# Optimization experiments

Measured on AMD Instinct MI355X. Metric: run time of the kernel, lower is better.

## Reference

```python
import jax, jax.numpy as jnp
import numpy as np

D_MODEL, D_FFN, N_EXPERTS, TOP_K = 1024, 4096, 8, 2
BATCH, SEQ = 4, 1024


def setup_inputs() -> dict:
    key = jax.random.key(0)
    kx, kr, k1, k2, k3 = jax.random.split(key, 5)
    scale = 0.02
    return {
        "x": jax.random.normal(kx, (BATCH, SEQ, D_MODEL), dtype=jnp.float32),
        "w_router": jax.random.normal(kr, (D_MODEL, N_EXPERTS), dtype=jnp.float32) * scale,
        "w1": jax.random.normal(k1, (N_EXPERTS, D_MODEL, D_FFN), dtype=jnp.float32) * scale,
        "w2": jax.random.normal(k2, (N_EXPERTS, D_FFN, D_MODEL), dtype=jnp.float32) * scale,
        "w3": jax.random.normal(k3, (N_EXPERTS, D_MODEL, D_FFN), dtype=jnp.float32) * scale,
    }


def reference(x, w_router, w1, w2, w3):
    B, S, D = x.shape
    E = w_router.shape[1]
    T = B * S
    xf = x.reshape(T, D)

    # --- router: softmax over experts, top-k, renormalize ---
    router_probs = jax.nn.softmax(xf @ w_router, axis=-1)          # (T, E)
    topk_probs, topk_idx = jax.lax.top_k(router_probs, TOP_K)      # (T, K)
    topk_probs = topk_probs / topk_probs.sum(axis=-1, keepdims=True)

    # per-token combine weight for each expert (top_k indices are distinct,
    # matching the torch per-slot accumulation exactly)
    comb = jnp.zeros((T, E), dtype=xf.dtype)
    comb = comb.at[jnp.arange(T)[:, None], topk_idx].add(topk_probs)  # (T, E)

    # --- dense SwiGLU experts (same math as masked loop) ---
    h = jnp.einsum("td,edf->tef", xf, w1)                          # (T, E, F)
    g = jnp.einsum("td,edf->tef", xf, w3)                          # (T, E, F)
    y = jnp.einsum("tef,efd->ted", jax.nn.silu(h) * g, w2)         # (T, E, D)
    out = jnp.einsum("te,ted->td", comb, y).reshape(B, S, D)

    # --- load-balance aux loss ---
    expert_mask = jax.nn.one_hot(topk_idx, E, dtype=jnp.float32).sum(axis=1)  # (T, E)
    tokens_per_expert = expert_mask.sum(axis=0) / T
    mean_probs = router_probs.mean(axis=0)
    aux_loss = E * jnp.sum(tokens_per_expert * mean_probs)
    return out, aux_loss
```

## Files before the change

kernel.cpp:

```cpp
#include <hip/hip_runtime.h>
#include <hip/hip_bf16.h>
#include <cstdint>
#include <cstddef>

#define TT 4096
#define DM 1024
#define DF 4096
#define NE 8
#define BTAB 72

typedef __attribute__((ext_vector_type(8))) short bf16x8;
typedef __attribute__((ext_vector_type(8))) unsigned short ushort8;
typedef __attribute__((ext_vector_type(4))) float f32x4;

static __device__ __forceinline__ unsigned short f2bf(float f) {
    union { float f; unsigned int u; } v; v.f = f;
    unsigned int u = v.u;
    return (unsigned short)((u + 0x7FFFu + ((u >> 16) & 1u)) >> 16);
}
static __device__ __forceinline__ float bf2f(unsigned short h) {
    union { unsigned int u; float f; } v; v.u = ((unsigned int)h) << 16;
    return v.f;
}

#define GLOAD16(gsrc, ldst)                                                        \
    __builtin_amdgcn_global_load_lds(                                              \
        (const __attribute__((address_space(1))) void*)(gsrc),                     \
        (__attribute__((address_space(3))) void*)(ldst), 16, 0, 0)

__global__ void transpose_to_bf16(const float* __restrict__ in,
                                  unsigned short* __restrict__ out,
                                  int R, int C) {
    __shared__ float tile[32][33];
    const int e = blockIdx.z;
    const float* src = in + (size_t)e * R * C;
    unsigned short* dst = out + (size_t)e * R * C;
    const int c0 = blockIdx.x * 32, r0 = blockIdx.y * 32;
    const int tx = threadIdx.x, ty = threadIdx.y;
    #pragma unroll
    for (int i = 0; i < 4; ++i) {
        int r = r0 + ty + i * 8;
        tile[ty + i * 8][tx] = src[(size_t)r * C + c0 + tx];
    }
    __syncthreads();
    #pragma unroll
    for (int i = 0; i < 4; ++i) {
        int c = c0 + ty + i * 8;
        dst[(size_t)c * R + r0 + tx] = f2bf(tile[tx][ty + i * 8]);
    }
}

__global__ void router_kernel(const float* __restrict__ x,
                              const float* __restrict__ wr,
                              unsigned short* __restrict__ xb,
                              int* __restrict__ topi, float* __restrict__ topw,
                              float* __restrict__ probsum) {
    __shared__ float s_ps[NE];
    const int tid = threadIdx.x;
    if (tid < NE) s_ps[tid] = 0.f;
    __syncthreads();
    const int wid = tid >> 6, lane = tid & 63;
    const int t = blockIdx.x * 4 + wid;
    float acc[NE] = {0.f, 0.f, 0.f, 0.f, 0.f, 0.f, 0.f, 0.f};
    const float* xr = x + (size_t)t * DM;
    unsigned short* xbr = xb + (size_t)t * DM;
    for (int it = 0; it < DM / 64; ++it) {
        int d = it * 64 + lane;
        float xv = xr[d];
        xbr[d] = f2bf(xv);
        const float* w = wr + d * NE;
        #pragma unroll
        for (int e = 0; e < NE; ++e) acc[e] = fmaf(xv, w[e], acc[e]);
    }
    #pragma unroll
    for (int e = 0; e < NE; ++e) {
        float v = acc[e];
        #pragma unroll
        for (int off = 32; off; off >>= 1) v += __shfl_xor(v, off);
        acc[e] = v;
    }
    if (lane == 0) {
        float m = acc[0];
        #pragma unroll
        for (int e = 1; e < NE; ++e) m = fmaxf(m, acc[e]);
        float p[NE], s = 0.f;
        #pragma unroll
        for (int e = 0; e < NE; ++e) { p[e] = expf(acc[e] - m); s += p[e]; }
        float inv = 1.f / s;
        #pragma unroll
        for (int e = 0; e < NE; ++e) { p[e] *= inv; atomicAdd(&s_ps[e], p[e]); }
        int i1 = 0; float p1 = p[0];
        #pragma unroll
        for (int e = 1; e < NE; ++e) if (p[e] > p1) { p1 = p[e]; i1 = e; }
        int i2 = -1; float p2 = -1.f;
        #pragma unroll
        for (int e = 0; e < NE; ++e) if (e != i1 && p[e] > p2) { p2 = p[e]; i2 = e; }
        float rs = 1.f / (p1 + p2);
        topi[t * 2] = i1; topi[t * 2 + 1] = i2;
        topw[t * 2] = p1 * rs; topw[t * 2 + 1] = p2 * rs;
    }
    __syncthreads();
    if (tid < NE) atomicAdd(&probsum[tid], s_ps[tid]);
}

__global__ void assign_kernel(const int* __restrict__ topi,
                              int* __restrict__ list, int* __restrict__ slotpos,
                              int* __restrict__ cnt) {
    const int e = blockIdx.x;
    __shared__ int s_wc[4];
    const int tid = threadIdx.x, wid = tid >> 6, lane = tid & 63;
    int running = 0;
    for (int base = 0; base < TT; base += 256) {
        int t = base + tid;
        int hit = 0, slot = 0;
        int a = topi[2 * t], b = topi[2 * t + 1];
        if (a == e) { hit = 1; slot = 0; }
        else if (b == e) { hit = 1; slot = 1; }
        unsigned long long m = __ballot(hit);
        if (lane == 0) s_wc[wid] = __popcll(m);
        __syncthreads();
        int pre = 0, tot = 0;
        #pragma unroll
        for (int q = 0; q < 4; ++q) { int c = s_wc[q]; tot += c; if (q < wid) pre += c; }
        if (hit) {
            int pos = running + pre + __popcll(m & ((1ull << lane) - 1ull));
            list[e * TT + pos] = t;
            slotpos[2 * t + slot] = pos;
        }
        running += tot;
        __syncthreads();
    }
    if (tid == 0) cnt[e] = running;
}

__global__ void finalize_kernel(const int* __restrict__ cnt,
                                const float* __restrict__ probsum,
                                int* __restrict__ offs,
                                unsigned int* __restrict__ blocktab,
                                float* __restrict__ out_aux) {
    int o = 0;
    float aux = 0.f;
    int nb = 0;
    for (int e = 0; e < NE; ++e) {
        offs[e] = o; o += cnt[e];
        aux += (float)cnt[e] * probsum[e];
        int nrb = (cnt[e] + 127) >> 7;
        for (int rb = 0; rb < nrb; ++rb) blocktab[nb++] = ((unsigned)e << 16) | rb;
    }
    while (nb < BTAB) blocktab[nb++] = 0xFFFFFFFFu;
    *out_aux = (float)NE * aux / ((float)TT * (float)TT);
}

static __device__ __forceinline__ const bf16x8* frag_ptr(
        const unsigned short* base, int row, int ph16) {
    return (const bf16x8*)((const char*)base + row * 64 + ph16);
}

__global__ __launch_bounds__(256, 2) void gemm1_kernel(
    const unsigned short* __restrict__ xb,
    const unsigned short* __restrict__ w1T,
    const unsigned short* __restrict__ w3T,
    unsigned short* __restrict__ act,
    const int* __restrict__ list,
    const int* __restrict__ cnt,
    const int* __restrict__ offs,
    const unsigned int* __restrict__ blocktab) {
    const unsigned int tab = blocktab[blockIdx.y];
    if (tab == 0xFFFFFFFFu) return;
    const int e = tab >> 16;
    const int rowbase = (int)(tab & 0xFFFFu) << 7;
    const int ce = cnt[e];
    const int fbase = blockIdx.x * 128;

    __shared__ __align__(16) unsigned short As[128 * 32];
    __shared__ __align__(16) unsigned short B1s[128 * 32];
    __shared__ __align__(16) unsigned short B3s[128 * 32];

    const int tid = threadIdx.x;
    const int lrow = tid >> 2;
    const int q = (tid & 3) ^ ((tid >> 3) & 3);

    int sp0 = rowbase + lrow;       if (sp0 >= ce) sp0 = ce - 1;
    int sp1 = rowbase + 64 + lrow;  if (sp1 >= ce) sp1 = ce - 1;
    const size_t tok0 = (size_t)list[e * TT + sp0];
    const size_t tok1 = (size_t)list[e * TT + sp1];

    const unsigned short* a0 = xb + tok0 * DM + q * 8;
    const unsigned short* a1 = xb + tok1 * DM + q * 8;
    const unsigned short* b1a = w1T + ((size_t)e * DF + fbase + lrow) * DM + q * 8;
    const unsigned short* b1b = b1a + (size_t)64 * DM;
    const unsigned short* b3a = w3T + ((size_t)e * DF + fbase + lrow) * DM + q * 8;
    const unsigned short* b3b = b3a + (size_t)64 * DM;

    char* ldsA  = (char*)As  + tid * 16;
    char* ldsB1 = (char*)B1s + tid * 16;
    char* ldsB3 = (char*)B3s + tid * 16;

    const int wid = tid >> 6, lane = tid & 63;
    const int wm = wid >> 1, wn = wid & 1;
    const int g = lane >> 4, r = lane & 15;
    const int ph16 = (g ^ ((r >> 1) & 3)) << 4;

    f32x4 acch[4][4] = {};
    f32x4 accg[4][4] = {};

    for (int k0 = 0; k0 < DM; k0 += 32) {
        GLOAD16(a0 + k0,  ldsA);
        GLOAD16(a1 + k0,  ldsA + 4096);
        GLOAD16(b1a + k0, ldsB1);
        GLOAD16(b1b + k0, ldsB1 + 4096);
        GLOAD16(b3a + k0, ldsB3);
        GLOAD16(b3b + k0, ldsB3 + 4096);
        __syncthreads();
        bf16x8 af[4];
        #pragma unroll
        for (int m = 0; m < 4; ++m)
            af[m] = *frag_ptr(As, wm * 64 + m * 16 + r, ph16);
        #pragma unroll
        for (int n = 0; n < 4; ++n) {
            bf16x8 f1 = *frag_ptr(B1s, wn * 64 + n * 16 + r, ph16);
            bf16x8 f3 = *frag_ptr(B3s, wn * 64 + n * 16 + r, ph16);
            #pragma unroll
            for (int m = 0; m < 4; ++m) {
                acch[m][n] = __builtin_amdgcn_mfma_f32_16x16x32_bf16(af[m], f1, acch[m][n], 0, 0, 0);
                accg[m][n] = __builtin_amdgcn_mfma_f32_16x16x32_bf16(af[m], f3, accg[m][n], 0, 0, 0);
            }
        }
        __syncthreads();
    }

    const int ob = offs[e];
    #pragma unroll
    for (int m = 0; m < 4; ++m) {
        #pragma unroll
        for (int j = 0; j < 4; ++j) {
            const int pos = rowbase + wm * 64 + m * 16 + g * 4 + j;
            if (pos < ce) {
                unsigned short* arow = act + (size_t)(ob + pos) * DF + fbase + wn * 64;
                #pragma unroll
                for (int n = 0; n < 4; ++n) {
                    float h = acch[m][n][j];
                    float gv = accg[m][n][j];
                    float a = (h / (1.f + __expf(-h))) * gv;
                    arow[n * 16 + r] = f2bf(a);
                }
            }
        }
    }
}

__global__ __launch_bounds__(256, 2) void gemm2_kernel(
    const unsigned short* __restrict__ act,
    const unsigned short* __restrict__ w2T,
    unsigned short* __restrict__ ybuf,
    const int* __restrict__ cnt,
    const int* __restrict__ offs,
    const unsigned int* __restrict__ blocktab) {
    const unsigned int tab = blocktab[blockIdx.y];
    if (tab == 0xFFFFFFFFu) return;
    const int e = tab >> 16;
    const int rowbase = (int)(tab & 0xFFFFu) << 7;
    const int ce = cnt[e];
    const int dbase = blockIdx.x * 128;
    const int ob = offs[e];

    __shared__ __align__(16) unsigned short As[128 * 32];
    __shared__ __align__(16) unsigned short Bs[128 * 32];

    const int tid = threadIdx.x;
    const int lrow = tid >> 2;
    const int q = (tid & 3) ^ ((tid >> 3) & 3);

    int sp0 = rowbase + lrow;       if (sp0 >= ce) sp0 = ce - 1;
    int sp1 = rowbase + 64 + lrow;  if (sp1 >= ce) sp1 = ce - 1;

    const unsigned short* a0 = act + (size_t)(ob + sp0) * DF + q * 8;
    const unsigned short* a1 = act + (size_t)(ob + sp1) * DF + q * 8;
    const unsigned short* b0 = w2T + ((size_t)e * DM + dbase + lrow) * DF + q * 8;
    const unsigned short* b1 = b0 + (size_t)64 * DF;

    char* ldsA = (char*)As + tid * 16;
    char* ldsB = (char*)Bs + tid * 16;

    const int wid = tid >> 6, lane = tid & 63;
    const int wm = wid >> 1, wn = wid & 1;
    const int g = lane >> 4, r = lane & 15;
    const int ph16 = (g ^ ((r >> 1) & 3)) << 4;

    f32x4 acc[4][4] = {};

    for (int k0 = 0; k0 < DF; k0 += 32) {
        GLOAD16(a0 + k0, ldsA);
        GLOAD16(a1 + k0, ldsA + 4096);
        GLOAD16(b0 + k0, ldsB);
        GLOAD16(b1 + k0, ldsB + 4096);
        __syncthreads();
        bf16x8 af[4];
        #pragma unroll
        for (int m = 0; m < 4; ++m)
            af[m] = *frag_ptr(As, wm * 64 + m * 16 + r, ph16);
        #pragma unroll
        for (int n = 0; n < 4; ++n) {
            bf16x8 bfr = *frag_ptr(Bs, wn * 64 + n * 16 + r, ph16);
            #pragma unroll
            for (int m = 0; m < 4; ++m)
                acc[m][n] = __builtin_amdgcn_mfma_f32_16x16x32_bf16(af[m], bfr, acc[m][n], 0, 0, 0);
        }
        __syncthreads();
    }

    #pragma unroll
    for (int m = 0; m < 4; ++m) {
        #pragma unroll
        for (int j = 0; j < 4; ++j) {
            const int pos = rowbase + wm * 64 + m * 16 + g * 4 + j;
            if (pos < ce) {
                unsigned short* yrow = ybuf + (size_t)(ob + pos) * DM + dbase + wn * 64;
                #pragma unroll
                for (int n = 0; n < 4; ++n)
                    yrow[n * 16 + r] = f2bf(acc[m][n][j]);
            }
        }
    }
}

__global__ void combine_kernel(const unsigned short* __restrict__ ybuf,
                               const int* __restrict__ topi,
                               const float* __restrict__ topw,
                               const int* __restrict__ slotpos,
                               const int* __restrict__ offs,
                               float* __restrict__ out) {
    const int t = blockIdx.x;
    const int tid = threadIdx.x;
    const int e0 = topi[2 * t], e1 = topi[2 * t + 1];
    const int r0 = offs[e0] + slotpos[2 * t];
    const int r1 = offs[e1] + slotpos[2 * t + 1];
    const float w0 = topw[2 * t], w1 = topw[2 * t + 1];
    ushort4 a = *(const ushort4*)(ybuf + (size_t)r0 * DM + tid * 4);
    ushort4 b = *(const ushort4*)(ybuf + (size_t)r1 * DM + tid * 4);
    float4 o;
    o.x = w0 * bf2f(a.x) + w1 * bf2f(b.x);
    o.y = w0 * bf2f(a.y) + w1 * bf2f(b.y);
    o.z = w0 * bf2f(a.z) + w1 * bf2f(b.z);
    o.w = w0 * bf2f(a.w) + w1 * bf2f(b.w);
    *(float4*)(out + (size_t)t * DM + tid * 4) = o;
}

extern "C" void kernel_launch(void* const* d_in, const int* in_sizes, int n_in,
                              void* d_out, int out_size, void* d_ws, size_t ws_size,
                              hipStream_t stream) {
    (void)in_sizes; (void)n_in; (void)ws_size;
    const float* x  = (const float*)d_in[0];
    const float* wr = (const float*)d_in[1];
    const float* w1 = (const float*)d_in[2];
    const float* w2 = (const float*)d_in[3];
    const float* w3 = (const float*)d_in[4];
    float* out = (float*)d_out;

    char* ws = (char*)d_ws;
    size_t off = 0;
    auto alloc = [&](size_t bytes) -> void* {
        void* p = ws + off;
        off = (off + bytes + 255) & ~(size_t)255;
        return p;
    };
    unsigned short* w1T = (unsigned short*)alloc((size_t)NE * DF * DM * 2);
    unsigned short* w3T = (unsigned short*)alloc((size_t)NE * DF * DM * 2);
    unsigned short* w2T = (unsigned short*)alloc((size_t)NE * DM * DF * 2);
    unsigned short* act = (unsigned short*)alloc((size_t)2 * TT * DF * 2);
    unsigned short* xb  = (unsigned short*)alloc((size_t)TT * DM * 2);
    int*   topi    = (int*)alloc(TT * 2 * sizeof(int));
    float* topw    = (float*)alloc(TT * 2 * sizeof(float));
    int*   list    = (int*)alloc((size_t)NE * TT * sizeof(int));
    int*   slotpos = (int*)alloc(TT * 2 * sizeof(int));
    int*   cnt     = (int*)alloc(NE * sizeof(int));
    int*   offs    = (int*)alloc(NE * sizeof(int));
    float* probsum = (float*)alloc(NE * sizeof(float));
    unsigned int* blocktab = (unsigned int*)alloc(BTAB * sizeof(unsigned int));
    unsigned short* ybuf = w1T;

    hipMemsetAsync(probsum, 0, NE * sizeof(float), stream);

    dim3 tb(32, 8);
    transpose_to_bf16<<<dim3(DF / 32, DM / 32, NE), tb, 0, stream>>>(w1, w1T, DM, DF);
    transpose_to_bf16<<<dim3(DF / 32, DM / 32, NE), tb, 0, stream>>>(w3, w3T, DM, DF);
    transpose_to_bf16<<<dim3(DM / 32, DF / 32, NE), tb, 0, stream>>>(w2, w2T, DF, DM);

    router_kernel<<<TT / 4, 256, 0, stream>>>(x, wr, xb, topi, topw, probsum);
    assign_kernel<<<NE, 256, 0, stream>>>(topi, list, slotpos, cnt);
    finalize_kernel<<<1, 1, 0, stream>>>(cnt, probsum, offs, blocktab, out + (out_size - 1));

    gemm1_kernel<<<dim3(DF / 128, BTAB), 256, 0, stream>>>(xb, w1T, w3T, act, list, cnt, offs, blocktab);
    gemm2_kernel<<<dim3(DM / 128, BTAB), 256, 0, stream>>>(act, w2T, ybuf, cnt, offs, blocktab);
    combine_kernel<<<TT, 256, 0, stream>>>(ybuf, topi, topw, slotpos, offs, out);
}
```

Baseline: 481.4 us.

## Triple-buffer GEMM K-loops with async LDS loads and vectorize weight transpose

Both expert GEMMs now use a three-stage LDS ring buffer. Global-to-LDS loads for tile t+2 are issued before computing tile t, and explicit vmcnt waits plus barriers replace the two __syncthreads per iteration, so memory latency can overlap with MFMA work. gemm2's launch bounds go up to 3 blocks per CU. The weight transpose/bf16 conversion kernel moves to 64x64 tiles with float4 loads and 16-byte ushort8 stores. The extra LDS (48KB for gemm1) can cut occupancy, and the hand-counted vmcnt values must stay correct for the number of loads per stage.

```diff
diff --git a/kernel.cpp b/kernel.cpp
--- a/kernel.cpp
+++ b/kernel.cpp
@@ -28,25 +28,34 @@
         (const __attribute__((address_space(1))) void*)(gsrc),                     \
         (__attribute__((address_space(3))) void*)(ldst), 16, 0, 0)
 
-__global__ void transpose_to_bf16(const float* __restrict__ in,
-                                  unsigned short* __restrict__ out,
-                                  int R, int C) {
-    __shared__ float tile[32][33];
+__global__ void transpose_v2(const float* __restrict__ in,
+                             unsigned short* __restrict__ out,
+                             int R, int C) {
+    __shared__ float tile[64][65];
     const int e = blockIdx.z;
     const float* src = in + (size_t)e * R * C;
     unsigned short* dst = out + (size_t)e * R * C;
-    const int c0 = blockIdx.x * 32, r0 = blockIdx.y * 32;
-    const int tx = threadIdx.x, ty = threadIdx.y;
+    const int c0 = blockIdx.x * 64, r0 = blockIdx.y * 64;
+    const int tid = threadIdx.x;
     #pragma unroll
     for (int i = 0; i < 4; ++i) {
-        int r = r0 + ty + i * 8;
-        tile[ty + i * 8][tx] = src[(size_t)r * C + c0 + tx];
+        int idx = tid + i * 256;
+        int rr = idx >> 4, cc = idx & 15;
+        float4 v = *(const float4*)(src + (size_t)(r0 + rr) * C + c0 + cc * 4);
+        tile[rr][cc * 4 + 0] = v.x;
+        tile[rr][cc * 4 + 1] = v.y;
+        tile[rr][cc * 4 + 2] = v.z;
+        tile[rr][cc * 4 + 3] = v.w;
     }
     __syncthreads();
     #pragma unroll
-    for (int i = 0; i < 4; ++i) {
-        int c = c0 + ty + i * 8;
-        dst[(size_t)c * R + r0 + tx] = f2bf(tile[tx][ty + i * 8]);
+    for (int i = 0; i < 2; ++i) {
+        int idx = tid + i * 256;
+        int c = idx >> 3, rc = idx & 7;
+        ushort8 o;
+        #pragma unroll
+        for (int j = 0; j < 8; ++j) o[j] = f2bf(tile[rc * 8 + j][c]);
+        *(ushort8*)(dst + (size_t)(c0 + c) * R + r0 + rc * 8) = o;
     }
 }
 
@@ -156,6 +165,13 @@
     return (const bf16x8*)((const char*)base + row * 64 + ph16);
 }
 
+#define WAITBAR(N)                                                \
+    asm volatile("s_waitcnt vmcnt(" #N ")" ::: "memory");         \
+    __builtin_amdgcn_s_barrier();
+#define ENDBAR                                                    \
+    asm volatile("" ::: "memory");                                \
+    __builtin_amdgcn_s_barrier();
+
 __global__ __launch_bounds__(256, 2) void gemm1_kernel(
     const unsigned short* __restrict__ xb,
     const unsigned short* __restrict__ w1T,
@@ -172,9 +188,9 @@
     const int ce = cnt[e];
     const int fbase = blockIdx.x * 128;
 
-    __shared__ __align__(16) unsigned short As[128 * 32];
-    __shared__ __align__(16) unsigned short B1s[128 * 32];
-    __shared__ __align__(16) unsigned short B3s[128 * 32];
+    __shared__ __align__(16) unsigned short As[3 * 128 * 32];
+    __shared__ __align__(16) unsigned short B1s[3 * 128 * 32];
+    __shared__ __align__(16) unsigned short B3s[3 * 128 * 32];
 
     const int tid = threadIdx.x;
     const int lrow = tid >> 2;
@@ -204,30 +220,50 @@
     f32x4 acch[4][4] = {};
     f32x4 accg[4][4] = {};
 
-    for (int k0 = 0; k0 < DM; k0 += 32) {
-        GLOAD16(a0 + k0,  ldsA);
-        GLOAD16(a1 + k0,  ldsA + 4096);
-        GLOAD16(b1a + k0, ldsB1);
-        GLOAD16(b1b + k0, ldsB1 + 4096);
-        GLOAD16(b3a + k0, ldsB3);
-        GLOAD16(b3b + k0, ldsB3 + 4096);
-        __syncthreads();
-        bf16x8 af[4];
-        #pragma unroll
-        for (int m = 0; m < 4; ++m)
-            af[m] = *frag_ptr(As, wm * 64 + m * 16 + r, ph16);
-        #pragma unroll
-        for (int n = 0; n < 4; ++n) {
-            bf16x8 f1 = *frag_ptr(B1s, wn * 64 + n * 16 + r, ph16);
-            bf16x8 f3 = *frag_ptr(B3s, wn * 64 + n * 16 + r, ph16);
-            #pragma unroll
-            for (int m = 0; m < 4; ++m) {
-                acch[m][n] = __builtin_amdgcn_mfma_f32_16x16x32_bf16(af[m], f1, acch[m][n], 0, 0, 0);
-                accg[m][n] = __builtin_amdgcn_mfma_f32_16x16x32_bf16(af[m], f3, accg[m][n], 0, 0, 0);
-            }
-        }
-        __syncthreads();
-    }
+#define STAGE1(T, BUF)                                   \
+    {   const int koff = (T) * 32;                       \
+        const int bo = (BUF) * 8192;                     \
+        GLOAD16(a0 + koff,  ldsA + bo);                  \
+        GLOAD16(a1 + koff,  ldsA + bo + 4096);           \
+        GLOAD16(b1a + koff, ldsB1 + bo);                 \
+        GLOAD16(b1b + koff, ldsB1 + bo + 4096);          \
+        GLOAD16(b3a + koff, ldsB3 + bo);                 \
+        GLOAD16(b3b + koff, ldsB3 + bo + 4096); }
+
+#define COMP1(BS)                                                           \
+    {   const unsigned short* Ac  = As  + (BS) * 4096;                      \
+        const unsigned short* B1c = B1s + (BS) * 4096;                      \
+        const unsigned short* B3c = B3s + (BS) * 4096;                      \
+        bf16x8 af[4];                                                       \
+        _Pragma("unroll") for (int m = 0; m < 4; ++m)                       \
+            af[m] = *frag_ptr(Ac, wm * 64 + m * 16 + r, ph16);              \
+        _Pragma("unroll") for (int n = 0; n < 4; ++n) {                     \
+            bf16x8 f1 = *frag_ptr(B1c, wn * 64 + n * 16 + r, ph16);         \
+            bf16x8 f3 = *frag_ptr(B3c, wn * 64 + n * 16 + r, ph16);         \
+            _Pragma("unroll") for (int m = 0; m < 4; ++m) {                 \
+                acch[m][n] = __builtin_amdgcn_mfma_f32_16x16x32_bf16(af[m], f1, acch[m][n], 0, 0, 0); \
+                accg[m][n] = __builtin_amdgcn_mfma_f32_16x16x32_bf16(af[m], f3, accg[m][n], 0, 0, 0); } } }
+
+    const int NT = DM / 32;
+    STAGE1(0, 0);
+    STAGE1(1, 1);
+    int bs = 0, sb = 2;
+    for (int t = 0; t < NT - 2; ++t) {
+        STAGE1(t + 2, sb);
+        WAITBAR(12)
+        COMP1(bs)
+        ENDBAR
+        bs = (bs + 1 == 3) ? 0 : bs + 1;
+        sb = (sb + 1 == 3) ? 0 : sb + 1;
+    }
+    WAITBAR(6)
+    COMP1(bs)
+    ENDBAR
+    bs = (bs + 1 == 3) ? 0 : bs + 1;
+    WAITBAR(0)
+    COMP1(bs)
+#undef STAGE1
+#undef COMP1
 
     const int ob = offs[e];
     #pragma unroll
@@ -249,7 +285,7 @@
     }
 }
 
-__global__ __launch_bounds__(256, 2) void gemm2_kernel(
+__global__ __launch_bounds__(256, 3) void gemm2_kernel(
     const unsigned short* __restrict__ act,
     const unsigned short* __restrict__ w2T,
     unsigned short* __restrict__ ybuf,
@@ -264,8 +300,8 @@
     const int dbase = blockIdx.x * 128;
     const int ob = offs[e];
 
-    __shared__ __align__(16) unsigned short As[128 * 32];
-    __shared__ __align__(16) unsigned short Bs[128 * 32];
+    __shared__ __align__(16) unsigned short As[3 * 128 * 32];
+    __shared__ __align__(16) unsigned short Bs[3 * 128 * 32];
 
     const int tid = threadIdx.x;
     const int lrow = tid >> 2;
@@ -289,25 +325,45 @@
 
     f32x4 acc[4][4] = {};
 
-    for (int k0 = 0; k0 < DF; k0 += 32) {
-        GLOAD16(a0 + k0, ldsA);
-        GLOAD16(a1 + k0, ldsA + 4096);
-        GLOAD16(b0 + k0, ldsB);
-        GLOAD16(b1 + k0, ldsB + 4096);
-        __syncthreads();
-        bf16x8 af[4];
-        #pragma unroll
-        for (int m = 0; m < 4; ++m)
-            af[m] = *frag_ptr(As, wm * 64 + m * 16 + r, ph16);
-        #pragma unroll
-        for (int n = 0; n < 4; ++n) {
-            bf16x8 bfr = *frag_ptr(Bs, wn * 64 + n * 16 + r, ph16);
-            #pragma unroll
-            for (int m = 0; m < 4; ++m)
-                acc[m][n] = __builtin_amdgcn_mfma_f32_16x16x32_bf16(af[m], bfr, acc[m][n], 0, 0, 0);
-        }
-        __syncthreads();
-    }
+#define STAGE2(T, BUF)                                   \
+    {   const int koff = (T) * 32;                       \
+        const int bo = (BUF) * 8192;                     \
+        GLOAD16(a0 + koff, ldsA + bo);                   \
+        GLOAD16(a1 + koff, ldsA + bo + 4096);            \
+        GLOAD16(b0 + koff, ldsB + bo);                   \
+        GLOAD16(b1 + koff, ldsB + bo + 4096); }
+
+#define COMP2(BS)                                                           \
+    {   const unsigned short* Ac = As + (BS) * 4096;                        \
+        const unsigned short* Bc = Bs + (BS) * 4096;                        \
+        bf16x8 af[4];                                                       \
+        _Pragma("unroll") for (int m = 0; m < 4; ++m)                       \
+            af[m] = *frag_ptr(Ac, wm * 64 + m * 16 + r, ph16);              \
+        _Pragma("unroll") for (int n = 0; n < 4; ++n) {                     \
+            bf16x8 bfr = *frag_ptr(Bc, wn * 64 + n * 16 + r, ph16);         \
+            _Pragma("unroll") for (int m = 0; m < 4; ++m)                   \
+                acc[m][n] = __builtin_amdgcn_mfma_f32_16x16x32_bf16(af[m], bfr, acc[m][n], 0, 0, 0); } }
+
+    const int NT = DF / 32;
+    STAGE2(0, 0);
+    STAGE2(1, 1);
+    int bs = 0, sb = 2;
+    for (int t = 0; t < NT - 2; ++t) {
+        STAGE2(t + 2, sb);
+        WAITBAR(8)
+        COMP2(bs)
+        ENDBAR
+        bs = (bs + 1 == 3) ? 0 : bs + 1;
+        sb = (sb + 1 == 3) ? 0 : sb + 1;
+    }
+    WAITBAR(4)
+    COMP2(bs)
+    ENDBAR
+    bs = (bs + 1 == 3) ? 0 : bs + 1;
+    WAITBAR(0)
+    COMP2(bs)
+#undef STAGE2
+#undef COMP2
 
     #pragma unroll
     for (int m = 0; m < 4; ++m) {
@@ -381,10 +437,10 @@
 
     hipMemsetAsync(probsum, 0, NE * sizeof(float), stream);
 
-    dim3 tb(32, 8);
-    transpose_to_bf16<<<dim3(DF / 32, DM / 32, NE), tb, 0, stream>>>(w1, w1T, DM, DF);
-    transpose_to_bf16<<<dim3(DF / 32, DM / 32, NE), tb, 0, stream>>>(w3, w3T, DM, DF);
-    transpose_to_bf16<<<dim3(DM / 32, DF / 32, NE), tb, 0, stream>>>(w2, w2T, DF, DM);
+    dim3 tb(256);
+    transpose_v2<<<dim3(DF / 64, DM / 64, NE), tb, 0, stream>>>(w1, w1T, DM, DF);
+    transpose_v2<<<dim3(DF / 64, DM / 64, NE), tb, 0, stream>>>(w3, w3T, DM, DF);
+    transpose_v2<<<dim3(DM / 64, DF / 64, NE), tb, 0, stream>>>(w2, w2T, DF, DM);
 
     router_kernel<<<TT / 4, 256, 0, stream>>>(x, wr, xb, topi, topw, probsum);
     assign_kernel<<<NE, 256, 0, stream>>>(topi, list, slotpos, cnt);
```

New measurement: 465.7 us. 3.3% less time.
